# Kernel tuning notes

Measured on AMD Instinct MI355X. Metric: run time of the kernel, lower is better.

Reference implementation:

```python
import jax, jax.numpy as jnp
import numpy as np

POOL_SIZE = 7


def _pool_matrix(dim_size: int, pool_size: int) -> np.ndarray:
    # Faithful to torch.linspace(0, dim, pool_size+1, dtype=torch.int):
    # float linspace then truncation toward zero.
    bins = np.linspace(0, dim_size, pool_size + 1).astype(np.int64)
    P = np.zeros((pool_size, dim_size), dtype=np.float32)
    for i in range(pool_size):
        s, e = int(bins[i]), int(bins[i + 1])
        P[i, s:e] = 1.0 / (e - s)
    return P


def setup_inputs() -> dict:
    key = jax.random.key(0)
    x = jax.random.normal(key, (32, 2048, 28, 28), dtype=jnp.float32)
    return {"x": x}


def reference(x) -> jnp.ndarray:
    B, C, H, W = x.shape
    Ph = jnp.asarray(_pool_matrix(H, POOL_SIZE))  # [P, H], row i averages bin i
    Pw = jnp.asarray(_pool_matrix(W, POOL_SIZE))  # [P, W]
    # out[b, i, j, c] = mean of x[b, c, h_bin_i, w_bin_j]
    out = jnp.einsum('bchw,ih,jw->bijc', x, Ph, Pw)  # [B, P, P, C]
    return out.reshape(B, POOL_SIZE * POOL_SIZE, C)  # [B, 49, C], matches torch stack order (i-major)
```

## Files before the change

kernel.cpp:

```cpp
#include <hip/hip_runtime.h>


#define CH 2048
#define BN 32
#define IMG_F4 196
#define OUT_PER_B (49 * CH)

__global__ __launch_bounds__(256) void upp_pool_kernel(const float* __restrict__ x,
                                                       float* __restrict__ out) {
    __shared__ float lds[4][200];

    const int wave = threadIdx.x >> 6;
    const int lane = threadIdx.x & 63;
    const int bc   = blockIdx.x * 4 + wave;

    const float4* img = (const float4*)(x + (size_t)bc * 784);
    float* myLds = lds[wave];

    #pragma unroll
    for (int k = 0; k < 3; ++k) {
        const int f = k * 64 + lane;
        const float4 v = img[f];
        myLds[f] = (v.x + v.y) + (v.z + v.w);
    }
    if (lane < 4) {
        const int f = 192 + lane;
        const float4 v = img[f];
        myLds[f] = (v.x + v.y) + (v.z + v.w);
    }

    __syncthreads();

    if (lane < 49) {
        const int i = lane / 7;
        const int j = lane - i * 7;
        const int base = i * 28 + j;
        const float s = (myLds[base] + myLds[base + 7]) +
                        (myLds[base + 14] + myLds[base + 21]);
        const int b = bc >> 11;
        const int c = bc & (CH - 1);
        out[(size_t)b * OUT_PER_B + lane * CH + c] = s * (1.0f / 16.0f);
    }
}

extern "C" void kernel_launch(void* const* d_in, const int* in_sizes, int n_in,
                              void* d_out, int out_size, void* d_ws, size_t ws_size,
                              hipStream_t stream) {
    const float* x = (const float*)d_in[0];
    float* out = (float*)d_out;

    const int n_images = BN * CH;
    const int blocks = n_images / 4;
    upp_pool_kernel<<<blocks, 256, 0, stream>>>(x, out);
}
```

Measured before the change: 284.3 us.

## Batch 64 channels per block and coalesce output writes through LDS transpose

Each block now processes 64 consecutive channels of one batch, with each wave looping over 16 images and staging pooled results in a shared buffer. The results are then written out as contiguous 64-float rows per pool position instead of strided single-float stores. This targets the uncoalesced scattered output writes. The cost is fewer blocks, serialized per-image loads and two block-wide barriers per iteration, which may reduce memory-level parallelism.

```diff
diff --git a/kernel.cpp b/kernel.cpp
--- a/kernel.cpp
+++ b/kernel.cpp
@@ -2,44 +2,53 @@
 
 
 #define CH 2048
-#define BN 32
-#define IMG_F4 196
 #define OUT_PER_B (49 * CH)
 
 __global__ __launch_bounds__(256) void upp_pool_kernel(const float* __restrict__ x,
                                                        float* __restrict__ out) {
-    __shared__ float lds[4][200];
+    __shared__ float scratch[4][200];
+    __shared__ float res[49][65];
 
     const int wave = threadIdx.x >> 6;
     const int lane = threadIdx.x & 63;
-    const int bc   = blockIdx.x * 4 + wave;
+    const int b    = blockIdx.x >> 5;
+    const int c0   = (blockIdx.x & 31) * 64;
 
-    const float4* img = (const float4*)(x + (size_t)bc * 784);
-    float* myLds = lds[wave];
+    float* myLds = scratch[wave];
+    const float* imgBase = x + ((size_t)b * CH + c0 + wave * 16) * 784;
 
-    #pragma unroll
-    for (int k = 0; k < 3; ++k) {
-        const int f = k * 64 + lane;
-        const float4 v = img[f];
-        myLds[f] = (v.x + v.y) + (v.z + v.w);
-    }
-    if (lane < 4) {
-        const int f = 192 + lane;
-        const float4 v = img[f];
-        myLds[f] = (v.x + v.y) + (v.z + v.w);
+    const int bi   = lane / 7;
+    const int bj   = lane - bi * 7;
+    const int bofs = bi * 28 + bj;
+
+    for (int it = 0; it < 16; ++it) {
+        const float4* img = (const float4*)(imgBase + (size_t)it * 784);
+
+        const float4 v0 = img[lane];
+        const float4 v1 = img[lane + 64];
+        const float4 v2 = img[lane + 128];
+        myLds[lane]       = (v0.x + v0.y) + (v0.z + v0.w);
+        myLds[lane + 64]  = (v1.x + v1.y) + (v1.z + v1.w);
+        myLds[lane + 128] = (v2.x + v2.y) + (v2.z + v2.w);
+        if (lane < 4) {
+            const float4 v3 = img[192 + lane];
+            myLds[192 + lane] = (v3.x + v3.y) + (v3.z + v3.w);
+        }
+
+        __syncthreads();
+
+        if (lane < 49) {
+            const float s = (myLds[bofs] + myLds[bofs + 7]) +
+                            (myLds[bofs + 14] + myLds[bofs + 21]);
+            res[lane][wave * 16 + it] = s * (1.0f / 16.0f);
+        }
+
+        __syncthreads();
     }
 
-    __syncthreads();
-
-    if (lane < 49) {
-        const int i = lane / 7;
-        const int j = lane - i * 7;
-        const int base = i * 28 + j;
-        const float s = (myLds[base] + myLds[base + 7]) +
-                        (myLds[base + 14] + myLds[base + 21]);
-        const int b = bc >> 11;
-        const int c = bc & (CH - 1);
-        out[(size_t)b * OUT_PER_B + lane * CH + c] = s * (1.0f / 16.0f);
+    float* outBase = out + (size_t)b * OUT_PER_B + c0;
+    for (int p = wave; p < 49; p += 4) {
+        outBase[(size_t)p * CH + lane] = res[p][lane];
     }
 }
 
@@ -49,7 +58,5 @@
     const float* x = (const float*)d_in[0];
     float* out = (float*)d_out;
 
-    const int n_images = BN * CH;
-    const int blocks = n_images / 4;
-    upp_pool_kernel<<<blocks, 256, 0, stream>>>(x, out);
+    upp_pool_kernel<<<1024, 256, 0, stream>>>(x, out);
 }
```

Measured after the change: 281.6 us. No clear change (-1.0%).
